# Performance work log

Hardware: AMD Instinct MI355X
Metric: run time of the kernel (lower is better)

## Reference

```python
import jax, jax.numpy as jnp
import numpy as np

SINKHORN_ITERS = 5
EPS_CLAMP = 1e-8   # matches torch eps=1e-08 in unbalanced_optimal_transport
EPS_COS = 1e-6     # matches cosine_distance eps
EPS_DIV = 1e-6     # matches weighted_ref / rigid transform eps


def setup_inputs() -> dict:
    key = jax.random.key(0)
    k0, k1, k2, k3 = jax.random.split(key, 4)
    B, D, M, N = 32, 512, 1024, 1024
    return {
        "src_embedding": jax.random.normal(k0, (B, D, M), dtype=jnp.float32),
        "tgt_embedding": jax.random.normal(k1, (B, D, N), dtype=jnp.float32),
        "src": jax.random.normal(k2, (B, 3, M), dtype=jnp.float32),
        "tgt": jax.random.normal(k3, (B, 3, N), dtype=jnp.float32),
        "l": jnp.float32(1.0),    # learned scalar nn.Parameter
        "rho": jnp.float32(1.0),  # learned scalar nn.Parameter
    }


def reference(src_embedding, tgt_embedding, src, tgt, l, rho):
    # ---- batched cosine distance: C[b] = 1 - <x1, x2> / (|x1||x2|) ----
    x1 = jnp.swapaxes(src_embedding, 1, 2)  # (B, M, D)
    x2 = jnp.swapaxes(tgt_embedding, 1, 2)  # (B, N, D)
    w1 = jnp.linalg.norm(x1, axis=2, keepdims=True)  # (B, M, 1)
    w2 = jnp.linalg.norm(x2, axis=2, keepdims=True)  # (B, N, 1)
    denom = jnp.clip(w1 * jnp.swapaxes(w2, 1, 2), EPS_COS, None)
    C = 1.0 - jnp.einsum('bmd,bnd->bmn', x1, x2) / denom  # (B, M, N)

    # ---- batched unbalanced Sinkhorn (5 fixed iterations) ----
    B, M, N = C.shape
    a = jnp.float32(1.0 / M)
    b = jnp.float32(1.0 / N)
    K = jnp.exp(-C / jnp.clip(l, EPS_CLAMP, None))        # (B, M, N)
    fi = rho / jnp.clip(rho + l, EPS_CLAMP, None)
    v = jnp.full((B, N), b, dtype=C.dtype)
    u = jnp.full((B, M), a, dtype=C.dtype)
    for _ in range(SINKHORN_ITERS):
        u = (a / jnp.clip(jnp.einsum('bmn,bn->bm', K, v), EPS_CLAMP, None)) ** fi
        v = (b / jnp.clip(jnp.einsum('bmn,bm->bn', K, u), EPS_CLAMP, None)) ** fi
    P = u[:, :, None] * K * v[:, None, :]                  # transport plan (B, M, N)

    # ---- soft correspondences ----
    row = jnp.sum(P, axis=2)                               # (B, M)
    tgt_pts = jnp.swapaxes(tgt, 1, 2)                      # (B, N, 3)
    weighted_ref = jnp.einsum('bmn,bnd->bmd', P, tgt_pts) / (row[:, :, None] + EPS_DIV)

    # ---- weighted Kabsch rigid transform (batched 3x3 SVD) ----
    a_pts = jnp.swapaxes(src, 1, 2)                        # (B, M, 3)
    w = row[:, :, None] / (jnp.sum(row, axis=1)[:, None, None] + EPS_DIV)  # (B, M, 1)
    centroid_a = jnp.sum(a_pts * w, axis=1)                # (B, 3)
    centroid_b = jnp.sum(weighted_ref * w, axis=1)         # (B, 3)
    a_c = a_pts - centroid_a[:, None, :]
    b_c = weighted_ref - centroid_b[:, None, :]
    cov = jnp.einsum('bmi,bmj->bij', a_c, b_c * w)         # (B, 3, 3)

    U, S, Vh = jnp.linalg.svd(cov, full_matrices=True)
    V = jnp.swapaxes(Vh, 1, 2)                             # torch.svd returns V, not V^T
    Ut = jnp.swapaxes(U, 1, 2)
    rot_pos = V @ Ut
    rot_neg = V.at[:, :, 2].multiply(-1.0) @ Ut            # flip last column of V
    det = jnp.linalg.det(rot_pos)[:, None, None]
    R = jnp.where(det > 0, rot_pos, rot_neg)               # (B, 3, 3)
    t = -jnp.einsum('bij,bj->bi', R, centroid_a) + centroid_b  # (B, 3)
    return R, t, P
```

## Files before the change

### kernel.cpp

```cpp
#include <hip/hip_runtime.h>
#include <math.h>

#define BB 32
#define DD 512
#define MM 1024
#define NN 1024

typedef float f32x4 __attribute__((ext_vector_type(4)));
typedef _Float16 f16x8 __attribute__((ext_vector_type(8)));


__global__ __launch_bounds__(256)
void norms_init_kernel(const float* __restrict__ srcE, const float* __restrict__ tgtE,
                       float* __restrict__ w1, float* __restrict__ w2,
                       float* __restrict__ v, float* __restrict__ colsum)
{
    const int idx = blockIdx.x * 256 + threadIdx.x;
    const float* e; float* w; int r;
    if (idx < 32768) {
        e = srcE; w = w1; r = idx;
        v[idx] = 1.0f / 1024.0f;
        colsum[idx] = 0.0f;
    } else {
        e = tgtE; w = w2; r = idx - 32768;
    }
    const int b = r >> 10;
    const int m = r & 1023;
    const float* p = e + (size_t)b * (DD * MM) + m;
    float acc = 0.f;
    #pragma unroll 8
    for (int d = 0; d < DD; ++d) {
        const float x = p[(size_t)d * MM];
        acc = fmaf(x, x, acc);
    }
    w[r] = sqrtf(acc);
}

__global__ __launch_bounds__(256)
void gemm_kexp_kernel(const float* __restrict__ Ae, const float* __restrict__ Be,
                      const float* __restrict__ w1, const float* __restrict__ w2,
                      const float* __restrict__ lp, float* __restrict__ Kout)
{
    __shared__ _Float16 As[128 * 64];
    __shared__ _Float16 Bs[128 * 64];

    const int tid  = threadIdx.x;
    const int lane = tid & 63;
    const int wave = tid >> 6;
    const int m0 = blockIdx.x * 128;
    const int n0 = blockIdx.y * 128;
    const int b  = blockIdx.z;
    const int wm = (wave & 1) * 64;
    const int wn = (wave >> 1) * 64;
    const int m16  = lane & 15;
    const int quad = lane >> 4;

    const float* Ab = Ae + (size_t)b * DD * MM;
    const float* Bb = Be + (size_t)b * DD * NN;

    f32x4 acc[4][4];
    #pragma unroll
    for (int i = 0; i < 4; ++i)
        #pragma unroll
        for (int j = 0; j < 4; ++j)
            acc[i][j] = (f32x4){0.f, 0.f, 0.f, 0.f};

    const int sm = tid & 127;
    const int kh = tid >> 7;
    const int sw = sm & 7;
    const float* apBase = Ab + m0 + sm;
    const float* bpBase = Bb + n0 + sm;

    float av[4][8], bv[4][8];
    #pragma unroll
    for (int t = 0; t < 4; ++t) {
        const int kg = kh + 2 * t;
        const float* ap = apBase + (size_t)(kg * 8) * MM;
        const float* bp = bpBase + (size_t)(kg * 8) * NN;
        #pragma unroll
        for (int j = 0; j < 8; ++j) { av[t][j] = ap[(size_t)j * MM]; bv[t][j] = bp[(size_t)j * NN]; }
    }

    for (int kt = 0; kt < 8; ++kt) {
        f16x8 pa[4], pb[4];
        #pragma unroll
        for (int t = 0; t < 4; ++t)
            #pragma unroll
            for (int j = 0; j < 8; ++j) { pa[t][j] = (_Float16)av[t][j]; pb[t][j] = (_Float16)bv[t][j]; }
        if (kt) __syncthreads();
        #pragma unroll
        for (int t = 0; t < 4; ++t) {
            const int kg = kh + 2 * t;
            const int off = sm * 64 + ((kg ^ sw) << 3);
            *reinterpret_cast<f16x8*>(&As[off]) = pa[t];
            *reinterpret_cast<f16x8*>(&Bs[off]) = pb[t];
        }
        __syncthreads();
        if (kt < 7) {
            const size_t kbase = (size_t)(kt + 1) * 64;
            #pragma unroll
            for (int t = 0; t < 4; ++t) {
                const int kg = kh + 2 * t;
                const float* ap = apBase + (kbase + kg * 8) * MM;
                const float* bp = bpBase + (kbase + kg * 8) * NN;
                #pragma unroll
                for (int j = 0; j < 8; ++j) { av[t][j] = ap[(size_t)j * MM]; bv[t][j] = bp[(size_t)j * NN]; }
            }
        }
        #pragma unroll
        for (int ks = 0; ks < 2; ++ks) {
            const int kg = ks * 4 + quad;
            f16x8 af[4], bfr[4];
            #pragma unroll
            for (int i = 0; i < 4; ++i) {
                const int rm = wm + i * 16 + m16;
                af[i]  = *reinterpret_cast<const f16x8*>(&As[rm * 64 + ((kg ^ (rm & 7)) << 3)]);
                const int rn = wn + i * 16 + m16;
                bfr[i] = *reinterpret_cast<const f16x8*>(&Bs[rn * 64 + ((kg ^ (rn & 7)) << 3)]);
            }
            #pragma unroll
            for (int i = 0; i < 4; ++i)
                #pragma unroll
                for (int j = 0; j < 4; ++j)
                    acc[i][j] = __builtin_amdgcn_mfma_f32_16x16x32_f16(af[i], bfr[j], acc[i][j], 0, 0, 0);
        }
    }

    const float inv_l = 1.0f / fmaxf(lp[0], 1e-8f);
    float w2v[4];
    #pragma unroll
    for (int j = 0; j < 4; ++j) w2v[j] = w2[b * NN + n0 + wn + j * 16 + m16];
    #pragma unroll
    for (int i = 0; i < 4; ++i) {
        #pragma unroll
        for (int r = 0; r < 4; ++r) {
            const int m = m0 + wm + i * 16 + quad * 4 + r;
            const float w1v = w1[b * MM + m];
            unsigned short* rowp =
                (unsigned short*)((char*)Kout + ((size_t)((b << 10) + m) << 12));
            #pragma unroll
            for (int j = 0; j < 4; ++j) {
                const float dot = acc[i][j][r];
                const float den = fmaxf(w1v * w2v[j], 1e-6f);
                const float kv  = __expf((dot / den - 1.0f) * inv_l);
                rowp[n0 + wn + j * 16 + m16] =
                    (unsigned short)fminf(fmaf(kv, 65535.0f, 0.5f), 65535.0f);
            }
        }
    }
}

__global__ __launch_bounds__(256)
void uv_fused_kernel(const float* __restrict__ Kmat, const float* __restrict__ v,
                     float* __restrict__ u, float* __restrict__ colsum,
                     const float* __restrict__ lp, const float* __restrict__ rp)
{
    const int ms = blockIdx.x;
    const int b  = blockIdx.y;
    const int wv = threadIdx.x >> 6, lane = threadIdx.x & 63;
    const float l = lp[0], rho = rp[0];
    const float fi = rho / fmaxf(rho + l, 1e-8f);
    const int m0 = ms * 32 + wv * 8;
    const int gid0 = (b << 10) + m0;

    uint4 ku[8][2];
    #pragma unroll
    for (int r = 0; r < 8; ++r) {
        const uint4* kr = (const uint4*)((const char*)Kmat + ((size_t)(gid0 + r) << 12));
        ku[r][0] = kr[lane];
        ku[r][1] = kr[64 + lane];
    }
    const float4* vb4 = (const float4*)(v + (b << 10));
    float4 vv[4];
    vv[0] = vb4[2 * lane];       vv[1] = vb4[2 * lane + 1];
    vv[2] = vb4[128 + 2 * lane]; vv[3] = vb4[129 + 2 * lane];

    float s[8];
    #pragma unroll
    for (int r = 0; r < 8; ++r) {
        float t = 0.f;
        #pragma unroll
        for (int c = 0; c < 2; ++c) {
            const uint4 q = ku[r][c];
            const float4 va = vv[2 * c], vb2 = vv[2 * c + 1];
            t = fmaf((float)(q.x & 0xffffu), va.x, t);
            t = fmaf((float)(q.x >> 16),     va.y, t);
            t = fmaf((float)(q.y & 0xffffu), va.z, t);
            t = fmaf((float)(q.y >> 16),     va.w, t);
            t = fmaf((float)(q.z & 0xffffu), vb2.x, t);
            t = fmaf((float)(q.z >> 16),     vb2.y, t);
            t = fmaf((float)(q.w & 0xffffu), vb2.z, t);
            t = fmaf((float)(q.w >> 16),     vb2.w, t);
        }
        s[r] = t;
    }
    #pragma unroll
    for (int off = 32; off > 0; off >>= 1)
        #pragma unroll
        for (int r = 0; r < 8; ++r) s[r] += __shfl_down(s[r], off);
    float um[8];
    #pragma unroll
    for (int r = 0; r < 8; ++r) {
        const float sv = __builtin_amdgcn_readfirstlane(s[r]) * (1.0f / 65535.0f);
        um[r] = __powf((1.0f / 1024.0f) / fmaxf(sv, 1e-8f), fi);
    }
    if (lane == 0) {
        float* ub = u + (b << 10);
        #pragma unroll
        for (int r = 0; r < 8; ++r) ub[m0 + r] = um[r];
    }

    float cacc[16];
    #pragma unroll
    for (int j = 0; j < 16; ++j) cacc[j] = 0.f;
    #pragma unroll
    for (int r = 0; r < 8; ++r) {
        const float umr = um[r];
        #pragma unroll
        for (int c = 0; c < 2; ++c) {
            const uint4 q = ku[r][c];
            float* cc = &cacc[8 * c];
            cc[0] = fmaf((float)(q.x & 0xffffu), umr, cc[0]);
            cc[1] = fmaf((float)(q.x >> 16),     umr, cc[1]);
            cc[2] = fmaf((float)(q.y & 0xffffu), umr, cc[2]);
            cc[3] = fmaf((float)(q.y >> 16),     umr, cc[3]);
            cc[4] = fmaf((float)(q.z & 0xffffu), umr, cc[4]);
            cc[5] = fmaf((float)(q.z >> 16),     umr, cc[5]);
            cc[6] = fmaf((float)(q.w & 0xffffu), umr, cc[6]);
            cc[7] = fmaf((float)(q.w >> 16),     umr, cc[7]);
        }
    }
    __shared__ float red[4][1024];
    *reinterpret_cast<float4*>(&red[wv][8 * lane])           = make_float4(cacc[0],  cacc[1],  cacc[2],  cacc[3]);
    *reinterpret_cast<float4*>(&red[wv][8 * lane + 4])       = make_float4(cacc[4],  cacc[5],  cacc[6],  cacc[7]);
    *reinterpret_cast<float4*>(&red[wv][512 + 8 * lane])     = make_float4(cacc[8],  cacc[9],  cacc[10], cacc[11]);
    *reinterpret_cast<float4*>(&red[wv][512 + 8 * lane + 4]) = make_float4(cacc[12], cacc[13], cacc[14], cacc[15]);
    __syncthreads();
    const int t = threadIdx.x;
    float4 s4 = *reinterpret_cast<const float4*>(&red[0][4 * t]);
    #pragma unroll
    for (int w = 1; w < 4; ++w) {
        const float4 rw = *reinterpret_cast<const float4*>(&red[w][4 * t]);
        s4.x += rw.x; s4.y += rw.y; s4.z += rw.z; s4.w += rw.w;
    }
    float* cs = colsum + (b << 10) + 4 * t;
    atomicAdd(cs + 0, s4.x);
    atomicAdd(cs + 1, s4.y);
    atomicAdd(cs + 2, s4.z);
    atomicAdd(cs + 3, s4.w);
}

__global__ __launch_bounds__(256)
void v_finalize_kernel(float* __restrict__ colsum, float* __restrict__ v,
                       const float* __restrict__ lp, const float* __restrict__ rp)
{
    const int idx = blockIdx.x * 256 + threadIdx.x;
    const float s = colsum[idx] * (1.0f / 65535.0f);
    colsum[idx] = 0.0f;
    const float l = lp[0], rho = rp[0];
    const float fi = rho / fmaxf(rho + l, 1e-8f);
    v[idx] = __powf((1.0f / 1024.0f) / fmaxf(s, 1e-8f), fi);
}

__global__ __launch_bounds__(256)
void p_pass_kernel(float* __restrict__ Kmat, const float* __restrict__ u,
                   const float* __restrict__ v, const float* __restrict__ tgt,
                   float* __restrict__ rowb, float* __restrict__ wref)
{
    const int gid  = (blockIdx.x * 256 + threadIdx.x) >> 6;
    const int lane = threadIdx.x & 63;
    const int b = gid >> 10;
    char* rowbase = (char*)Kmat + ((size_t)gid << 12);
    const uint4* kr = (const uint4*)rowbase;
    uint4 ku[2];
    ku[0] = kr[lane];
    ku[1] = kr[64 + lane];
    const float4* vb = (const float4*)(v + (b << 10));
    const float4* tb = (const float4*)(tgt + (size_t)b * 3072);
    const float um_s = u[gid] * (1.0f / 65535.0f);
    float4 vv[4], txa[4], tya[4], tza[4];
    vv[0]  = vb[2 * lane];        vv[1]  = vb[2 * lane + 1];
    vv[2]  = vb[128 + 2 * lane];  vv[3]  = vb[129 + 2 * lane];
    txa[0] = tb[2 * lane];        txa[1] = tb[2 * lane + 1];
    txa[2] = tb[128 + 2 * lane];  txa[3] = tb[129 + 2 * lane];
    tya[0] = tb[256 + 2 * lane];  tya[1] = tb[257 + 2 * lane];
    tya[2] = tb[384 + 2 * lane];  tya[3] = tb[385 + 2 * lane];
    tza[0] = tb[512 + 2 * lane];  tza[1] = tb[513 + 2 * lane];
    tza[2] = tb[640 + 2 * lane];  tza[3] = tb[641 + 2 * lane];
    asm volatile("s_waitcnt vmcnt(0)" ::: "memory");
    float4* prow = (float4*)rowbase;
    float s = 0.f, x = 0.f, y = 0.f, z = 0.f;
    #pragma unroll
    for (int c = 0; c < 2; ++c) {
        const uint4 q = ku[c];
        const float k0 = (float)(q.x & 0xffffu), k1 = (float)(q.x >> 16);
        const float k2 = (float)(q.y & 0xffffu), k3 = (float)(q.y >> 16);
        const float k4 = (float)(q.z & 0xffffu), k5 = (float)(q.z >> 16);
        const float k6 = (float)(q.w & 0xffffu), k7 = (float)(q.w >> 16);
        const float4 va = vv[2 * c], vb2 = vv[2 * c + 1];
        float4 pa, pb;
        pa.x = um_s * k0 * va.x;  pa.y = um_s * k1 * va.y;
        pa.z = um_s * k2 * va.z;  pa.w = um_s * k3 * va.w;
        pb.x = um_s * k4 * vb2.x; pb.y = um_s * k5 * vb2.y;
        pb.z = um_s * k6 * vb2.z; pb.w = um_s * k7 * vb2.w;
        prow[c * 128 + 2 * lane]     = pa;
        prow[c * 128 + 2 * lane + 1] = pb;
        s += (pa.x + pa.y) + (pa.z + pa.w) + (pb.x + pb.y) + (pb.z + pb.w);
        const float4 x0 = txa[2 * c], x1 = txa[2 * c + 1];
        const float4 y0 = tya[2 * c], y1 = tya[2 * c + 1];
        const float4 z0 = tza[2 * c], z1 = tza[2 * c + 1];
        x = fmaf(pa.x, x0.x, x); x = fmaf(pa.y, x0.y, x);
        x = fmaf(pa.z, x0.z, x); x = fmaf(pa.w, x0.w, x);
        x = fmaf(pb.x, x1.x, x); x = fmaf(pb.y, x1.y, x);
        x = fmaf(pb.z, x1.z, x); x = fmaf(pb.w, x1.w, x);
        y = fmaf(pa.x, y0.x, y); y = fmaf(pa.y, y0.y, y);
        y = fmaf(pa.z, y0.z, y); y = fmaf(pa.w, y0.w, y);
        y = fmaf(pb.x, y1.x, y); y = fmaf(pb.y, y1.y, y);
        y = fmaf(pb.z, y1.z, y); y = fmaf(pb.w, y1.w, y);
        z = fmaf(pa.x, z0.x, z); z = fmaf(pa.y, z0.y, z);
        z = fmaf(pa.z, z0.z, z); z = fmaf(pa.w, z0.w, z);
        z = fmaf(pb.x, z1.x, z); z = fmaf(pb.y, z1.y, z);
        z = fmaf(pb.z, z1.z, z); z = fmaf(pb.w, z1.w, z);
    }
    #pragma unroll
    for (int off = 32; off > 0; off >>= 1) {
        s += __shfl_down(s, off);
        x += __shfl_down(x, off);
        y += __shfl_down(y, off);
        z += __shfl_down(z, off);
    }
    if (lane == 0) {
        rowb[gid] = s;
        const float inv = 1.0f / (s + 1e-6f);
        wref[gid * 3 + 0] = x * inv;
        wref[gid * 3 + 1] = y * inv;
        wref[gid * 3 + 2] = z * inv;
    }
}

__device__ __forceinline__ float block_reduce_sum(float x, float* lds4, int wv, int lane)
{
    #pragma unroll
    for (int off = 32; off > 0; off >>= 1) x += __shfl_down(x, off);
    __syncthreads();
    if (lane == 0) lds4[wv] = x;
    __syncthreads();
    return (lds4[0] + lds4[1]) + (lds4[2] + lds4[3]);
}

__global__ __launch_bounds__(256)
void kabsch_stats_kernel(const float* __restrict__ rowb, const float* __restrict__ wref,
                         const float* __restrict__ src, float* __restrict__ cov,
                         float* __restrict__ ca, float* __restrict__ cb)
{
    __shared__ float lds4[4];
    const int b = blockIdx.x, tid = threadIdx.x;
    const int wv = tid >> 6, lane = tid & 63;
    float r[4], w[4], ax[4], ay[4], az[4], bx[4], by[4], bz[4];
    float rsum = 0.f;
    #pragma unroll
    for (int i = 0; i < 4; ++i) {
        const int m = tid + 256 * i;
        r[i] = rowb[(b << 10) + m];
        rsum += r[i];
    }
    const float total = block_reduce_sum(rsum, lds4, wv, lane);
    const float inv = 1.0f / (total + 1e-6f);
    #pragma unroll
    for (int i = 0; i < 4; ++i) {
        const int m = tid + 256 * i;
        w[i]  = r[i] * inv;
        ax[i] = src[b * 3072 + m];
        ay[i] = src[b * 3072 + 1024 + m];
        az[i] = src[b * 3072 + 2048 + m];
        bx[i] = wref[((b << 10) + m) * 3 + 0];
        by[i] = wref[((b << 10) + m) * 3 + 1];
        bz[i] = wref[((b << 10) + m) * 3 + 2];
    }
    float cax = 0, cay = 0, caz = 0, cbx = 0, cby = 0, cbz = 0;
    #pragma unroll
    for (int i = 0; i < 4; ++i) {
        cax = fmaf(ax[i], w[i], cax); cay = fmaf(ay[i], w[i], cay); caz = fmaf(az[i], w[i], caz);
        cbx = fmaf(bx[i], w[i], cbx); cby = fmaf(by[i], w[i], cby); cbz = fmaf(bz[i], w[i], cbz);
    }
    cax = block_reduce_sum(cax, lds4, wv, lane);
    cay = block_reduce_sum(cay, lds4, wv, lane);
    caz = block_reduce_sum(caz, lds4, wv, lane);
    cbx = block_reduce_sum(cbx, lds4, wv, lane);
    cby = block_reduce_sum(cby, lds4, wv, lane);
    cbz = block_reduce_sum(cbz, lds4, wv, lane);
    float c[9] = {0,0,0,0,0,0,0,0,0};
    #pragma unroll
    for (int i = 0; i < 4; ++i) {
        const float dax = ax[i] - cax, day = ay[i] - cay, daz = az[i] - caz;
        const float dbx = (bx[i] - cbx) * w[i];
        const float dby = (by[i] - cby) * w[i];
        const float dbz = (bz[i] - cbz) * w[i];
        c[0] = fmaf(dax, dbx, c[0]); c[1] = fmaf(dax, dby, c[1]); c[2] = fmaf(dax, dbz, c[2]);
        c[3] = fmaf(day, dbx, c[3]); c[4] = fmaf(day, dby, c[4]); c[5] = fmaf(day, dbz, c[5]);
        c[6] = fmaf(daz, dbx, c[6]); c[7] = fmaf(daz, dby, c[7]); c[8] = fmaf(daz, dbz, c[8]);
    }
    #pragma unroll
    for (int k = 0; k < 9; ++k) c[k] = block_reduce_sum(c[k], lds4, wv, lane);
    if (tid == 0) {
        #pragma unroll
        for (int k = 0; k < 9; ++k) cov[b * 9 + k] = c[k];
        ca[b * 3 + 0] = cax; ca[b * 3 + 1] = cay; ca[b * 3 + 2] = caz;
        cb[b * 3 + 0] = cbx; cb[b * 3 + 1] = cby; cb[b * 3 + 2] = cbz;
    }
}

__device__ __forceinline__ void jrot_d(double S[3][3], double V[3][3], int p, int q)
{
    const double apq = S[p][q];
    if (fabs(apq) < 1e-300) return;
    const double theta = (S[q][q] - S[p][p]) / (2.0 * apq);
    const double tt = copysign(1.0, theta) / (fabs(theta) + sqrt(1.0 + theta * theta));
    const double c = 1.0 / sqrt(1.0 + tt * tt);
    const double s = tt * c;
    #pragma unroll
    for (int k = 0; k < 3; ++k) {
        const double skp = S[k][p], skq = S[k][q];
        S[k][p] = c * skp - s * skq;
        S[k][q] = s * skp + c * skq;
    }
    #pragma unroll
    for (int k = 0; k < 3; ++k) {
        const double spk = S[p][k], sqk = S[q][k];
        S[p][k] = c * spk - s * sqk;
        S[q][k] = s * spk + c * sqk;
    }
    #pragma unroll
    for (int k = 0; k < 3; ++k) {
        const double vkp = V[k][p], vkq = V[k][q];
        V[k][p] = c * vkp - s * vkq;
        V[k][q] = s * vkp + c * vkq;
    }
}

__global__ __launch_bounds__(64)
void svd_kernel(const float* __restrict__ cov, const float* __restrict__ ca,
                const float* __restrict__ cb, float* __restrict__ out)
{
    const int b = threadIdx.x;
    if (b >= 32) return;
    double A[3][3];
    #pragma unroll
    for (int i = 0; i < 3; ++i)
        #pragma unroll
        for (int j = 0; j < 3; ++j)
            A[i][j] = (double)cov[b * 9 + i * 3 + j];
    double S[3][3];
    #pragma unroll
    for (int i = 0; i < 3; ++i)
        #pragma unroll
        for (int j = 0; j < 3; ++j)
            S[i][j] = A[0][i] * A[0][j] + A[1][i] * A[1][j] + A[2][i] * A[2][j];
    double V[3][3] = {{1,0,0},{0,1,0},{0,0,1}};
    for (int sweep = 0; sweep < 8; ++sweep) {
        jrot_d(S, V, 0, 1);
        jrot_d(S, V, 0, 2);
        jrot_d(S, V, 1, 2);
    }
    int o0 = 0, o1 = 1, o2 = 2;
    double e0 = S[0][0], e1 = S[1][1], e2 = S[2][2];
    double tf; int ti;
    if (e0 < e1) { tf = e0; e0 = e1; e1 = tf; ti = o0; o0 = o1; o1 = ti; }
    if (e0 < e2) { tf = e0; e0 = e2; e2 = tf; ti = o0; o0 = o2; o2 = ti; }
    if (e1 < e2) { tf = e1; e1 = e2; e2 = tf; ti = o1; o1 = o2; o2 = ti; }
    double v1[3] = {V[0][o0], V[1][o0], V[2][o0]};
    double v2[3] = {V[0][o1], V[1][o1], V[2][o1]};
    double v3[3] = {V[0][o2], V[1][o2], V[2][o2]};
    double Av1[3], Av2[3];
    #pragma unroll
    for (int i = 0; i < 3; ++i) {
        Av1[i] = A[i][0] * v1[0] + A[i][1] * v1[1] + A[i][2] * v1[2];
        Av2[i] = A[i][0] * v2[0] + A[i][1] * v2[1] + A[i][2] * v2[2];
    }
    const double n1 = sqrt(Av1[0]*Av1[0] + Av1[1]*Av1[1] + Av1[2]*Av1[2]);
    const double in1 = 1.0 / fmax(n1, 1e-300);
    double u1[3] = {Av1[0]*in1, Av1[1]*in1, Av1[2]*in1};
    const double d12 = Av2[0]*u1[0] + Av2[1]*u1[1] + Av2[2]*u1[2];
    double u2[3] = {Av2[0] - d12*u1[0], Av2[1] - d12*u1[1], Av2[2] - d12*u1[2]};
    const double n2 = sqrt(u2[0]*u2[0] + u2[1]*u2[1] + u2[2]*u2[2]);
    const double in2 = 1.0 / fmax(n2, 1e-300);
    u2[0] *= in2; u2[1] *= in2; u2[2] *= in2;
    double u3[3] = {u1[1]*u2[2] - u1[2]*u2[1],
                    u1[2]*u2[0] - u1[0]*u2[2],
                    u1[0]*u2[1] - u1[1]*u2[0]};
    double R0[3][3];
    #pragma unroll
    for (int i = 0; i < 3; ++i)
        #pragma unroll
        for (int j = 0; j < 3; ++j)
            R0[i][j] = v1[i]*u1[j] + v2[i]*u2[j] + v3[i]*u3[j];
    const double det =
        R0[0][0]*(R0[1][1]*R0[2][2] - R0[1][2]*R0[2][1])
      - R0[0][1]*(R0[1][0]*R0[2][2] - R0[1][2]*R0[2][0])
      + R0[0][2]*(R0[1][0]*R0[2][1] - R0[1][1]*R0[2][0]);
    double Rm[3][3];
    if (det > 0.0) {
        #pragma unroll
        for (int i = 0; i < 3; ++i)
            #pragma unroll
            for (int j = 0; j < 3; ++j)
                Rm[i][j] = R0[i][j];
    } else {
        #pragma unroll
        for (int i = 0; i < 3; ++i)
            #pragma unroll
            for (int j = 0; j < 3; ++j)
                Rm[i][j] = R0[i][j] - 2.0 * v3[i] * u3[j];
    }
    const double cax = (double)ca[b*3+0], cay = (double)ca[b*3+1], caz = (double)ca[b*3+2];
    #pragma unroll
    for (int i = 0; i < 3; ++i)
        #pragma unroll
        for (int j = 0; j < 3; ++j)
            out[b * 9 + i * 3 + j] = (float)Rm[i][j];
    #pragma unroll
    for (int i = 0; i < 3; ++i)
        out[288 + b * 3 + i] = (float)((double)cb[b*3+i] - (Rm[i][0]*cax + Rm[i][1]*cay + Rm[i][2]*caz));
}

extern "C" void kernel_launch(void* const* d_in, const int* in_sizes, int n_in,
                              void* d_out, int out_size, void* d_ws, size_t ws_size,
                              hipStream_t stream)
{
    const float* srcE = (const float*)d_in[0];
    const float* tgtE = (const float*)d_in[1];
    const float* src  = (const float*)d_in[2];
    const float* tgt  = (const float*)d_in[3];
    const float* lp   = (const float*)d_in[4];
    const float* rp   = (const float*)d_in[5];
    float* out  = (float*)d_out;
    float* Pout = out + 384;

    float* ws     = (float*)d_ws;
    float* w1     = ws;
    float* w2     = ws + 32768;
    float* u      = ws + 65536;
    float* v      = ws + 98304;
    float* rowb   = ws + 131072;
    float* wref   = ws + 163840;
    float* colsum = ws + 262144;
    float* cov    = ws + 294912;
    float* ca     = ws + 295200;
    float* cb     = ws + 295296;

    norms_init_kernel<<<256, 256, 0, stream>>>(srcE, tgtE, w1, w2, v, colsum);
    gemm_kexp_kernel<<<dim3(8, 8, 32), 256, 0, stream>>>(srcE, tgtE, w1, w2, lp, Pout);
    for (int it = 0; it < 5; ++it) {
        uv_fused_kernel<<<dim3(32, 32), 256, 0, stream>>>(Pout, v, u, colsum, lp, rp);
        v_finalize_kernel<<<128, 256, 0, stream>>>(colsum, v, lp, rp);
    }
    p_pass_kernel<<<8192, 256, 0, stream>>>(Pout, u, v, tgt, rowb, wref);
    kabsch_stats_kernel<<<32, 256, 0, stream>>>(rowb, wref, src, cov, ca, cb);
    svd_kernel<<<1, 64, 0, stream>>>(cov, ca, cb, out);
}
```

Before: 553.2 us.

## Pre-transpose embeddings to fp16 scratch and double-buffer GEMM with direct-to-LDS loads

A new prep kernel computes the norms with coalesced float4 reads. It also writes a transposed fp16 copy of both embeddings into the unused upper half of each output row. The GEMM then fills a double-buffered shared-memory tile with global_load_lds from that copy, so the per-tile fp32 loads and fp16 conversions in registers go away and loads overlap with MFMA work. The K epilogue is staged through swizzled shared memory so rows are written with wide, coalesced stores. This adds an extra write and read of the fp16 copy and relies on the scratch half of the P buffer not being touched before the GEMM finishes.

```diff
diff --git a/kernel.cpp b/kernel.cpp
--- a/kernel.cpp
+++ b/kernel.cpp
@@ -11,38 +11,78 @@
 
 
 __global__ __launch_bounds__(256)
-void norms_init_kernel(const float* __restrict__ srcE, const float* __restrict__ tgtE,
-                       float* __restrict__ w1, float* __restrict__ w2,
-                       float* __restrict__ v, float* __restrict__ colsum)
-{
-    const int idx = blockIdx.x * 256 + threadIdx.x;
-    const float* e; float* w; int r;
-    if (idx < 32768) {
-        e = srcE; w = w1; r = idx;
+void prep_kernel(const float* __restrict__ srcE, const float* __restrict__ tgtE,
+                 float* __restrict__ w1, float* __restrict__ w2,
+                 float* __restrict__ v, float* __restrict__ colsum,
+                 float* __restrict__ Pout)
+{
+    __shared__ float T[64][65];
+    __shared__ float nsum[64];
+    const int mc  = blockIdx.x;
+    const int mat = blockIdx.y;
+    const int b   = blockIdx.z;
+    const int tid = threadIdx.x;
+    const float* E = mat ? tgtE : srcE;
+    float* w = mat ? w2 : w1;
+
+    if (tid < 64) nsum[tid] = 0.f;
+    if (mat == 0 && tid < 64) {
+        const int idx = ((b << 4) + mc) * 64 + tid;
         v[idx] = 1.0f / 1024.0f;
         colsum[idx] = 0.0f;
-    } else {
-        e = tgtE; w = w2; r = idx - 32768;
-    }
-    const int b = r >> 10;
-    const int m = r & 1023;
-    const float* p = e + (size_t)b * (DD * MM) + m;
-    float acc = 0.f;
-    #pragma unroll 8
-    for (int d = 0; d < DD; ++d) {
-        const float x = p[(size_t)d * MM];
-        acc = fmaf(x, x, acc);
-    }
-    w[r] = sqrtf(acc);
+    }
+
+    const int m4  = (tid & 15) * 4;
+    const int din = tid >> 4;
+    const int m0g = mc * 64;
+    const float* Eb = E + (size_t)b * (DD * MM) + m0g;
+
+    const int row = tid >> 2;
+    const int dc4 = tid & 3;
+    const int Rrow = mat * 32768 + b * 1024 + m0g + row;
+    char* obase = (char*)Pout + (((size_t)(Rrow >> 1)) << 12) + 2048
+                + ((size_t)(Rrow & 1) << 10);
+
+    float nacc[4] = {0.f, 0.f, 0.f, 0.f};
+
+    for (int p = 0; p < 8; ++p) {
+        const int d0 = p * 64;
+        __syncthreads();
+        float4 ld[4];
+        #pragma unroll
+        for (int s = 0; s < 4; ++s) {
+            const int d = d0 + din + 16 * s;
+            ld[s] = *reinterpret_cast<const float4*>(Eb + (size_t)d * MM + m4);
+        }
+        #pragma unroll
+        for (int s = 0; s < 4; ++s) {
+            nacc[0] = fmaf(ld[s].x, ld[s].x, nacc[0]);
+            nacc[1] = fmaf(ld[s].y, ld[s].y, nacc[1]);
+            nacc[2] = fmaf(ld[s].z, ld[s].z, nacc[2]);
+            nacc[3] = fmaf(ld[s].w, ld[s].w, nacc[3]);
+            *reinterpret_cast<float4*>(&T[din + 16 * s][m4]) = ld[s];
+        }
+        __syncthreads();
+        __attribute__((aligned(16))) _Float16 h[16];
+        #pragma unroll
+        for (int k = 0; k < 16; ++k) h[k] = (_Float16)T[dc4 * 16 + k][row];
+        *reinterpret_cast<f16x8*>(obase + (size_t)(d0 + dc4 * 16) * 2)
+            = *reinterpret_cast<f16x8*>(&h[0]);
+        *reinterpret_cast<f16x8*>(obase + (size_t)(d0 + dc4 * 16 + 8) * 2)
+            = *reinterpret_cast<f16x8*>(&h[8]);
+    }
+    #pragma unroll
+    for (int q = 0; q < 4; ++q) atomicAdd(&nsum[m4 + q], nacc[q]);
+    __syncthreads();
+    if (tid < 64) w[b * 1024 + m0g + tid] = sqrtf(nsum[tid]);
 }
 
 __global__ __launch_bounds__(256)
-void gemm_kexp_kernel(const float* __restrict__ Ae, const float* __restrict__ Be,
-                      const float* __restrict__ w1, const float* __restrict__ w2,
+void gemm_kexp_kernel(const float* __restrict__ w1, const float* __restrict__ w2,
                       const float* __restrict__ lp, float* __restrict__ Kout)
 {
-    __shared__ _Float16 As[128 * 64];
-    __shared__ _Float16 Bs[128 * 64];
+    __shared__ _Float16 As[2][8192];
+    __shared__ _Float16 Bs[2][8192];
 
     const int tid  = threadIdx.x;
     const int lane = tid & 63;
@@ -55,8 +95,21 @@
     const int m16  = lane & 15;
     const int quad = lane >> 4;
 
-    const float* Ab = Ae + (size_t)b * DD * MM;
-    const float* Bb = Be + (size_t)b * DD * NN;
+    const char* pbase = (const char*)Kout;
+    const char* srcA[4]; const char* srcB[4];
+    #pragma unroll
+    for (int c = 0; c < 4; ++c) {
+        const int idx  = (wave * 4 + c) * 64 + lane;
+        const int m    = idx >> 3;
+        const int kg   = idx & 7;
+        const int colb = ((kg ^ (m & 7)) << 4);
+        const int Ra = b * 1024 + m0 + m;
+        srcA[c] = pbase + (((size_t)(Ra >> 1)) << 12) + 2048
+                + ((size_t)(Ra & 1) << 10) + colb;
+        const int Rb = 32768 + b * 1024 + n0 + m;
+        srcB[c] = pbase + (((size_t)(Rb >> 1)) << 12) + 2048
+                + ((size_t)(Rb & 1) << 10) + colb;
+    }
 
     f32x4 acc[4][4];
     #pragma unroll
@@ -65,48 +118,26 @@
         for (int j = 0; j < 4; ++j)
             acc[i][j] = (f32x4){0.f, 0.f, 0.f, 0.f};
 
-    const int sm = tid & 127;
-    const int kh = tid >> 7;
-    const int sw = sm & 7;
-    const float* apBase = Ab + m0 + sm;
-    const float* bpBase = Bb + n0 + sm;
-
-    float av[4][8], bv[4][8];
-    #pragma unroll
-    for (int t = 0; t < 4; ++t) {
-        const int kg = kh + 2 * t;
-        const float* ap = apBase + (size_t)(kg * 8) * MM;
-        const float* bp = bpBase + (size_t)(kg * 8) * NN;
-        #pragma unroll
-        for (int j = 0; j < 8; ++j) { av[t][j] = ap[(size_t)j * MM]; bv[t][j] = bp[(size_t)j * NN]; }
-    }
-
+    auto stage = [&](int buf, int kt_) {
+        const int kb = kt_ * 128;
+        #pragma unroll
+        for (int c = 0; c < 4; ++c) {
+            __builtin_amdgcn_global_load_lds(
+                (const __attribute__((address_space(1))) unsigned int*)(srcA[c] + kb),
+                (__attribute__((address_space(3))) unsigned int*)&As[buf][(wave * 4 + c) * 512],
+                16, 0, 0);
+            __builtin_amdgcn_global_load_lds(
+                (const __attribute__((address_space(1))) unsigned int*)(srcB[c] + kb),
+                (__attribute__((address_space(3))) unsigned int*)&Bs[buf][(wave * 4 + c) * 512],
+                16, 0, 0);
+        }
+    };
+
+    stage(0, 0);
+    __syncthreads();
+    int cur = 0;
     for (int kt = 0; kt < 8; ++kt) {
-        f16x8 pa[4], pb[4];
-        #pragma unroll
-        for (int t = 0; t < 4; ++t)
-            #pragma unroll
-            for (int j = 0; j < 8; ++j) { pa[t][j] = (_Float16)av[t][j]; pb[t][j] = (_Float16)bv[t][j]; }
-        if (kt) __syncthreads();
-        #pragma unroll
-        for (int t = 0; t < 4; ++t) {
-            const int kg = kh + 2 * t;
-            const int off = sm * 64 + ((kg ^ sw) << 3);
-            *reinterpret_cast<f16x8*>(&As[off]) = pa[t];
-            *reinterpret_cast<f16x8*>(&Bs[off]) = pb[t];
-        }
-        __syncthreads();
-        if (kt < 7) {
-            const size_t kbase = (size_t)(kt + 1) * 64;
-            #pragma unroll
-            for (int t = 0; t < 4; ++t) {
-                const int kg = kh + 2 * t;
-                const float* ap = apBase + (kbase + kg * 8) * MM;
-                const float* bp = bpBase + (kbase + kg * 8) * NN;
-                #pragma unroll
-                for (int j = 0; j < 8; ++j) { av[t][j] = ap[(size_t)j * MM]; bv[t][j] = bp[(size_t)j * NN]; }
-            }
-        }
+        if (kt < 7) stage(cur ^ 1, kt + 1);
         #pragma unroll
         for (int ks = 0; ks < 2; ++ks) {
             const int kg = ks * 4 + quad;
@@ -114,9 +145,9 @@
             #pragma unroll
             for (int i = 0; i < 4; ++i) {
                 const int rm = wm + i * 16 + m16;
-                af[i]  = *reinterpret_cast<const f16x8*>(&As[rm * 64 + ((kg ^ (rm & 7)) << 3)]);
+                af[i]  = *reinterpret_cast<const f16x8*>(&As[cur][rm * 64 + ((kg ^ (rm & 7)) << 3)]);
                 const int rn = wn + i * 16 + m16;
-                bfr[i] = *reinterpret_cast<const f16x8*>(&Bs[rn * 64 + ((kg ^ (rn & 7)) << 3)]);
+                bfr[i] = *reinterpret_cast<const f16x8*>(&Bs[cur][rn * 64 + ((kg ^ (rn & 7)) << 3)]);
             }
             #pragma unroll
             for (int i = 0; i < 4; ++i)
@@ -124,29 +155,42 @@
                 for (int j = 0; j < 4; ++j)
                     acc[i][j] = __builtin_amdgcn_mfma_f32_16x16x32_f16(af[i], bfr[j], acc[i][j], 0, 0, 0);
         }
+        __syncthreads();
+        cur ^= 1;
     }
 
     const float inv_l = 1.0f / fmaxf(lp[0], 1e-8f);
     float w2v[4];
     #pragma unroll
     for (int j = 0; j < 4; ++j) w2v[j] = w2[b * NN + n0 + wn + j * 16 + m16];
+    unsigned short* Ls = (unsigned short*)&As[0][0];
     #pragma unroll
     for (int i = 0; i < 4; ++i) {
         #pragma unroll
         for (int r = 0; r < 4; ++r) {
-            const int m = m0 + wm + i * 16 + quad * 4 + r;
-            const float w1v = w1[b * MM + m];
-            unsigned short* rowp =
-                (unsigned short*)((char*)Kout + ((size_t)((b << 10) + m) << 12));
+            const int m = wm + i * 16 + quad * 4 + r;
+            const float w1v = w1[b * MM + m0 + m];
             #pragma unroll
             for (int j = 0; j < 4; ++j) {
                 const float dot = acc[i][j][r];
                 const float den = fmaxf(w1v * w2v[j], 1e-6f);
                 const float kv  = __expf((dot / den - 1.0f) * inv_l);
-                rowp[n0 + wn + j * 16 + m16] =
-                    (unsigned short)fminf(fmaf(kv, 65535.0f, 0.5f), 65535.0f);
+                const int n = wn + j * 16 + m16;
+                const int sidx = m * 128 + ((((n >> 3) ^ (m & 7)) << 3) | (n & 7));
+                Ls[sidx] = (unsigned short)fminf(fmaf(kv, 65535.0f, 0.5f), 65535.0f);
             }
         }
+    }
+    __syncthreads();
+    const int row = tid >> 1, half = tid & 1;
+    char* orow = (char*)Kout + ((size_t)(b * 1024 + m0 + row) << 12)
+               + (size_t)n0 * 2 + half * 128;
+    #pragma unroll
+    for (int c = 0; c < 8; ++c) {
+        const int g = half * 8 + c;
+        const uint4 val = *reinterpret_cast<const uint4*>(
+            &Ls[row * 128 + ((g ^ (row & 7)) << 3)]);
+        reinterpret_cast<uint4*>(orow)[c] = val;
     }
 }
 
@@ -548,8 +592,8 @@
     float* ca     = ws + 295200;
     float* cb     = ws + 295296;
 
-    norms_init_kernel<<<256, 256, 0, stream>>>(srcE, tgtE, w1, w2, v, colsum);
-    gemm_kexp_kernel<<<dim3(8, 8, 32), 256, 0, stream>>>(srcE, tgtE, w1, w2, lp, Pout);
+    prep_kernel<<<dim3(16, 2, 32), 256, 0, stream>>>(srcE, tgtE, w1, w2, v, colsum, Pout);
+    gemm_kexp_kernel<<<dim3(8, 8, 32), 256, 0, stream>>>(w1, w2, lp, Pout);
     for (int it = 0; it < 5; ++it) {
         uv_fused_kernel<<<dim3(32, 32), 256, 0, stream>>>(Pout, v, u, colsum, lp, rp);
         v_finalize_kernel<<<128, 256, 0, stream>>>(colsum, v, lp, rp);
```

Result: faster. 535.4 us (-3.2%).
